# Kernel optimization log

Measured on AMD Instinct MI355X. Metric: run time of the kernel, lower is better.

## Reference

```python
import jax, jax.numpy as jnp
import numpy as np

INPUT_SCALE = 1.0
TABLE_SIZE = 32
D_EMBED = 64
N = 1_000_000


def setup_inputs() -> dict:
    key = jax.random.key(0)
    k1, k2 = jax.random.split(key)
    x = jax.random.normal(k1, (N, 3), dtype=jnp.float32)
    # learned table parameter: [E, D, H, W] (batch dim of 1 dropped)
    table = jax.random.normal(k2, (D_EMBED, TABLE_SIZE, TABLE_SIZE, TABLE_SIZE), dtype=jnp.float32) * 0.1
    return {"x": x, "table": table}


def _grid_sample_3d(table, grid):
    """F.grid_sample(table[None], grid[None,None,None]) with mode='bilinear',
    padding_mode='zeros', align_corners=False.
    table: [E, D, H, W]; grid: [n, 3] with (x->W, y->H, z->D) order.
    Returns [n, E]."""
    E, Dz, Hy, Wx = table.shape
    sizes_f = jnp.array([Wx, Hy, Dz], dtype=table.dtype)
    dims_i = jnp.array([Wx, Hy, Dz], dtype=jnp.int32)
    # align_corners=False: pix = ((coord + 1) * size - 1) / 2
    pix = ((grid + 1.0) * sizes_f - 1.0) * 0.5   # [n, 3]
    p0f = jnp.floor(pix)
    frac = pix - p0f                              # [n, 3]
    p0 = p0f.astype(jnp.int32)
    tab_flat = table.reshape(E, -1).T             # [D*H*W, E]
    out = jnp.zeros((grid.shape[0], E), dtype=table.dtype)
    for dz in (0, 1):
        for dy in (0, 1):
            for dx in (0, 1):
                off = jnp.array([dx, dy, dz], dtype=jnp.int32)
                idx = p0 + off                                        # [n, 3]
                inb = jnp.all((idx >= 0) & (idx < dims_i), axis=-1)   # zeros padding
                idxc = jnp.clip(idx, 0, dims_i - 1)
                lin = (idxc[:, 2] * Hy + idxc[:, 1]) * Wx + idxc[:, 0]
                vals = tab_flat[lin]                                  # [n, E]
                w = jnp.prod(jnp.where(off == 1, frac, 1.0 - frac), axis=-1)
                out = out + vals * (w * inb.astype(table.dtype))[:, None]
    return out


def reference(x, table):
    xc = jnp.clip(x * INPUT_SCALE, -1.0, 1.0)
    return _grid_sample_3d(table, xc)
```

## Files before the change

### kernel.cpp

```cpp
#include <hip/hip_runtime.h>


constexpr int TSZ = 32;
constexpr int S   = TSZ * TSZ * TSZ;
constexpr int EMB = 64;

typedef float        floatx4 __attribute__((ext_vector_type(4)));
typedef float        f32x2   __attribute__((ext_vector_type(2)));

__device__ __forceinline__ unsigned short f32_to_bf16_rne(float f) {
  unsigned int u = __float_as_uint(f);
  unsigned int lsb = (u >> 16) & 1u;
  u += 0x7FFFu + lsb;
  return (unsigned short)(u >> 16);
}

__global__ __launch_bounds__(256) void transpose_table_k(
    const float* __restrict__ tab, unsigned short* __restrict__ tabT) {
  __shared__ float tile[EMB][EMB + 1];
  const int s_base = blockIdx.x * 64;
  const int t  = threadIdx.x;
  const int c0 = t & 63;
  const int r0 = t >> 6;
#pragma unroll
  for (int i = 0; i < 16; ++i) {
    const int e = r0 + 4 * i;
    tile[e][c0] = tab[(size_t)e * S + (s_base + c0)];
  }
  __syncthreads();
#pragma unroll
  for (int i = 0; i < 16; ++i) {
    const int s = r0 + 4 * i;
    tabT[(size_t)(s_base + s) * EMB + c0] = f32_to_bf16_rne(tile[c0][s]);
  }
}

__global__ __launch_bounds__(256) void embed_k(
    const float* __restrict__ x, const uint4* __restrict__ tabT,
    float* __restrict__ out, int n) {
  const int gid = blockIdx.x * 256 + threadIdx.x;
  const int pt  = gid >> 3;
  if (pt >= n) return;
  const int c8 = gid & 7;

  const float gx = fminf(fmaxf(__builtin_nontemporal_load(&x[3 * pt + 0]), -1.f), 1.f);
  const float gy = fminf(fmaxf(__builtin_nontemporal_load(&x[3 * pt + 1]), -1.f), 1.f);
  const float gz = fminf(fmaxf(__builtin_nontemporal_load(&x[3 * pt + 2]), -1.f), 1.f);
  const float px = ((gx + 1.f) * 32.f - 1.f) * 0.5f;
  const float py = ((gy + 1.f) * 32.f - 1.f) * 0.5f;
  const float pz = ((gz + 1.f) * 32.f - 1.f) * 0.5f;

  const float fxf = floorf(px), fyf = floorf(py), fzf = floorf(pz);
  const int ix0 = (int)fxf, iy0 = (int)fyf, iz0 = (int)fzf;
  const float fx = px - fxf, fy = py - fyf, fz = pz - fzf;

  float wxe[2], wye[2], wze[2];
  int   ixc[2], iyc[2], izc[2];
  wxe[0] = (ix0 >= 0)      ? (1.f - fx) : 0.f;
  wxe[1] = (ix0 + 1 < TSZ) ? fx         : 0.f;
  ixc[0] = max(ix0, 0);
  ixc[1] = min(ix0 + 1, TSZ - 1);
  wye[0] = (iy0 >= 0)      ? (1.f - fy) : 0.f;
  wye[1] = (iy0 + 1 < TSZ) ? fy         : 0.f;
  iyc[0] = max(iy0, 0);
  iyc[1] = min(iy0 + 1, TSZ - 1);
  wze[0] = (iz0 >= 0)      ? (1.f - fz) : 0.f;
  wze[1] = (iz0 + 1 < TSZ) ? fz         : 0.f;
  izc[0] = max(iz0, 0);
  izc[1] = min(iz0 + 1, TSZ - 1);

  f32x2 a01 = {0.f, 0.f}, a23 = {0.f, 0.f}, a45 = {0.f, 0.f}, a67 = {0.f, 0.f};

#pragma unroll
  for (int dz = 0; dz < 2; ++dz) {
    const int zb = izc[dz] * (TSZ * TSZ);
#pragma unroll
    for (int dy = 0; dy < 2; ++dy) {
      const int   zyb = zb + iyc[dy] * TSZ;
      const float wzy = wze[dz] * wye[dy];
#pragma unroll
      for (int dx = 0; dx < 2; ++dx) {
        const float w   = wzy * wxe[dx];
        const int   lin = zyb + ixc[dx];
        const uint4 q   = tabT[lin * 8 + c8];
        const f32x2 w2  = {w, w};
        const f32x2 v01 = {__uint_as_float(q.x << 16),
                           __uint_as_float(q.x & 0xFFFF0000u)};
        const f32x2 v23 = {__uint_as_float(q.y << 16),
                           __uint_as_float(q.y & 0xFFFF0000u)};
        const f32x2 v45 = {__uint_as_float(q.z << 16),
                           __uint_as_float(q.z & 0xFFFF0000u)};
        const f32x2 v67 = {__uint_as_float(q.w << 16),
                           __uint_as_float(q.w & 0xFFFF0000u)};
        a01 = __builtin_elementwise_fma(v01, w2, a01);
        a23 = __builtin_elementwise_fma(v23, w2, a23);
        a45 = __builtin_elementwise_fma(v45, w2, a45);
        a67 = __builtin_elementwise_fma(v67, w2, a67);
      }
    }
  }

  const float accv[8] = {a01.x, a01.y, a23.x, a23.y, a45.x, a45.y, a67.x, a67.y};
  const int lane = threadIdx.x & 63;
  const int grp  = lane & ~7;
  const int src1 = grp + (c8 >> 1);
  const int src2 = grp + 4 + (c8 >> 1);
  const bool hi  = (c8 & 1) != 0;
  float o0[4], o1[4];
#pragma unroll
  for (int j = 0; j < 4; ++j) {
    const float aj = __shfl(accv[j],     src1, 64);
    const float bj = __shfl(accv[4 + j], src1, 64);
    o0[j] = hi ? bj : aj;
    const float cj = __shfl(accv[j],     src2, 64);
    const float dj = __shfl(accv[4 + j], src2, 64);
    o1[j] = hi ? dj : cj;
  }
  const floatx4 s0 = {o0[0], o0[1], o0[2], o0[3]};
  const floatx4 s1 = {o1[0], o1[1], o1[2], o1[3]};
  float* rowp = out + (size_t)pt * EMB;
  *(floatx4*)(rowp + c8 * 4)      = s0;
  *(floatx4*)(rowp + 32 + c8 * 4) = s1;
}

__global__ __launch_bounds__(256) void embed_fallback_k(
    const float* __restrict__ x, const float* __restrict__ tab,
    float* __restrict__ out, int n) {
  const int gid = blockIdx.x * 256 + threadIdx.x;
  const int pt  = gid >> 6;
  if (pt >= n) return;
  const int e = gid & 63;

  const float gx = fminf(fmaxf(x[3 * pt + 0], -1.f), 1.f);
  const float gy = fminf(fmaxf(x[3 * pt + 1], -1.f), 1.f);
  const float gz = fminf(fmaxf(x[3 * pt + 2], -1.f), 1.f);
  const float px = ((gx + 1.f) * 32.f - 1.f) * 0.5f;
  const float py = ((gy + 1.f) * 32.f - 1.f) * 0.5f;
  const float pz = ((gz + 1.f) * 32.f - 1.f) * 0.5f;

  const float fxf = floorf(px), fyf = floorf(py), fzf = floorf(pz);
  const int ix0 = (int)fxf, iy0 = (int)fyf, iz0 = (int)fzf;
  const float fx = px - fxf, fy = py - fyf, fz = pz - fzf;
  const float wx[2] = {1.f - fx, fx};
  const float wy[2] = {1.f - fy, fy};
  const float wz[2] = {1.f - fz, fz};

  float acc = 0.f;
#pragma unroll
  for (int dz = 0; dz < 2; ++dz) {
    const int  iz  = iz0 + dz;
    const bool bz  = (unsigned)iz < (unsigned)TSZ;
    const int  izc = min(max(iz, 0), TSZ - 1);
#pragma unroll
    for (int dy = 0; dy < 2; ++dy) {
      const int  iy  = iy0 + dy;
      const bool by  = (unsigned)iy < (unsigned)TSZ;
      const int  iyc = min(max(iy, 0), TSZ - 1);
#pragma unroll
      for (int dx = 0; dx < 2; ++dx) {
        const int  ix  = ix0 + dx;
        const bool bx  = (unsigned)ix < (unsigned)TSZ;
        const int  ixc = min(max(ix, 0), TSZ - 1);
        float w = wz[dz] * wy[dy] * wx[dx];
        w = (bx && by && bz) ? w : 0.f;
        const int lin = (izc * TSZ + iyc) * TSZ + ixc;
        acc = fmaf(w, tab[(size_t)e * S + lin], acc);
      }
    }
  }
  out[(size_t)pt * EMB + e] = acc;
}

extern "C" void kernel_launch(void* const* d_in, const int* in_sizes, int n_in,
                              void* d_out, int out_size, void* d_ws,
                              size_t ws_size, hipStream_t stream) {
  const float* x   = (const float*)d_in[0];
  const float* tab = (const float*)d_in[1];
  float*       out = (float*)d_out;
  const int n = in_sizes[0] / 3;

  const size_t need = (size_t)S * EMB * sizeof(unsigned short);
  if (ws_size >= need) {
    unsigned short* tabT = (unsigned short*)d_ws;
    transpose_table_k<<<S / 64, 256, 0, stream>>>(tab, tabT);
    const int total  = n * 8;
    const int blocks = (total + 255) / 256;
    embed_k<<<blocks, 256, 0, stream>>>(x, (const uint4*)tabT, out, n);
  } else {
    const int total  = n * EMB;
    const int blocks = (total + 255) / 256;
    embed_fallback_k<<<blocks, 256, 0, stream>>>(x, tab, out, n);
  }
}
```

Before: 313.9 us.

## Quantize transposed table to int8 with per-channel scales for gathers

Adds a per-channel absmax pass and stores the transposed table as offset int8 (128-biased) instead of bf16. The embed kernel gathers 8 bytes per lane per corner, accumulates the weighted unsigned values, and then subtracts the bias and applies the scale, which halves table gather bytes. Output stores are switched to nontemporal. This adds an extra small kernel launch and lowers table precision to 8 bits, which may exceed the accuracy tolerance.

```diff
diff --git a/kernel.cpp b/kernel.cpp
--- a/kernel.cpp
+++ b/kernel.cpp
@@ -5,18 +5,28 @@
 constexpr int S   = TSZ * TSZ * TSZ;
 constexpr int EMB = 64;
 
-typedef float        floatx4 __attribute__((ext_vector_type(4)));
-typedef float        f32x2   __attribute__((ext_vector_type(2)));
-
-__device__ __forceinline__ unsigned short f32_to_bf16_rne(float f) {
-  unsigned int u = __float_as_uint(f);
-  unsigned int lsb = (u >> 16) & 1u;
-  u += 0x7FFFu + lsb;
-  return (unsigned short)(u >> 16);
-}
-
-__global__ __launch_bounds__(256) void transpose_table_k(
-    const float* __restrict__ tab, unsigned short* __restrict__ tabT) {
+typedef float floatx4 __attribute__((ext_vector_type(4)));
+
+__global__ __launch_bounds__(256) void amax_k(
+    const float* __restrict__ tab, float* __restrict__ scale) {
+  __shared__ float red[256];
+  const int ch = blockIdx.x;
+  const int t  = threadIdx.x;
+  float m = 0.f;
+  for (int i = 0; i < S / 256; ++i)
+    m = fmaxf(m, fabsf(tab[(size_t)ch * S + t + 256 * i]));
+  red[t] = m;
+  __syncthreads();
+  for (int off = 128; off > 0; off >>= 1) {
+    if (t < off) red[t] = fmaxf(red[t], red[t + off]);
+    __syncthreads();
+  }
+  if (t == 0) scale[ch] = fmaxf(red[0], 1e-30f) * (1.0f / 127.0f);
+}
+
+__global__ __launch_bounds__(256) void transpose_quant_k(
+    const float* __restrict__ tab, const float* __restrict__ scale,
+    unsigned char* __restrict__ tabQ) {
   __shared__ float tile[EMB][EMB + 1];
   const int s_base = blockIdx.x * 64;
   const int t  = threadIdx.x;
@@ -28,16 +38,18 @@
     tile[e][c0] = tab[(size_t)e * S + (s_base + c0)];
   }
   __syncthreads();
+  const float rs = 1.0f / scale[c0];
 #pragma unroll
   for (int i = 0; i < 16; ++i) {
     const int s = r0 + 4 * i;
-    tabT[(size_t)(s_base + s) * EMB + c0] = f32_to_bf16_rne(tile[c0][s]);
-  }
-}
-
-__global__ __launch_bounds__(256) void embed_k(
-    const float* __restrict__ x, const uint4* __restrict__ tabT,
-    float* __restrict__ out, int n) {
+    const int q = __float2int_rn(tile[c0][s] * rs) + 128;
+    tabQ[(size_t)(s_base + s) * EMB + c0] = (unsigned char)q;
+  }
+}
+
+__global__ __launch_bounds__(256) void embed_q_k(
+    const float* __restrict__ x, const unsigned char* __restrict__ tabQ,
+    const float* __restrict__ scale, float* __restrict__ out, int n) {
   const int gid = blockIdx.x * 256 + threadIdx.x;
   const int pt  = gid >> 3;
   if (pt >= n) return;
@@ -69,7 +81,9 @@
   izc[0] = max(iz0, 0);
   izc[1] = min(iz0 + 1, TSZ - 1);
 
-  f32x2 a01 = {0.f, 0.f}, a23 = {0.f, 0.f}, a45 = {0.f, 0.f}, a67 = {0.f, 0.f};
+  float a0 = 0.f, a1 = 0.f, a2 = 0.f, a3 = 0.f;
+  float a4 = 0.f, a5 = 0.f, a6 = 0.f, a7 = 0.f;
+  float sumw = 0.f;
 
 #pragma unroll
   for (int dz = 0; dz < 2; ++dz) {
@@ -82,25 +96,28 @@
       for (int dx = 0; dx < 2; ++dx) {
         const float w   = wzy * wxe[dx];
         const int   lin = zyb + ixc[dx];
-        const uint4 q   = tabT[lin * 8 + c8];
-        const f32x2 w2  = {w, w};
-        const f32x2 v01 = {__uint_as_float(q.x << 16),
-                           __uint_as_float(q.x & 0xFFFF0000u)};
-        const f32x2 v23 = {__uint_as_float(q.y << 16),
-                           __uint_as_float(q.y & 0xFFFF0000u)};
-        const f32x2 v45 = {__uint_as_float(q.z << 16),
-                           __uint_as_float(q.z & 0xFFFF0000u)};
-        const f32x2 v67 = {__uint_as_float(q.w << 16),
-                           __uint_as_float(q.w & 0xFFFF0000u)};
-        a01 = __builtin_elementwise_fma(v01, w2, a01);
-        a23 = __builtin_elementwise_fma(v23, w2, a23);
-        a45 = __builtin_elementwise_fma(v45, w2, a45);
-        a67 = __builtin_elementwise_fma(v67, w2, a67);
+        const uint2 q   = *(const uint2*)(tabQ + (size_t)lin * EMB + c8 * 8);
+        sumw += w;
+        a0 = fmaf(w, (float)(q.x & 0xFFu),         a0);
+        a1 = fmaf(w, (float)((q.x >> 8)  & 0xFFu), a1);
+        a2 = fmaf(w, (float)((q.x >> 16) & 0xFFu), a2);
+        a3 = fmaf(w, (float)((q.x >> 24) & 0xFFu), a3);
+        a4 = fmaf(w, (float)(q.y & 0xFFu),         a4);
+        a5 = fmaf(w, (float)((q.y >> 8)  & 0xFFu), a5);
+        a6 = fmaf(w, (float)((q.y >> 16) & 0xFFu), a6);
+        a7 = fmaf(w, (float)((q.y >> 24) & 0xFFu), a7);
       }
     }
   }
 
-  const float accv[8] = {a01.x, a01.y, a23.x, a23.y, a45.x, a45.y, a67.x, a67.y};
+  const float m128 = 128.0f * sumw;
+  const floatx4 sA = *(const floatx4*)(scale + c8 * 8);
+  const floatx4 sB = *(const floatx4*)(scale + c8 * 8 + 4);
+  const float accv[8] = {sA.x * (a0 - m128), sA.y * (a1 - m128),
+                         sA.z * (a2 - m128), sA.w * (a3 - m128),
+                         sB.x * (a4 - m128), sB.y * (a5 - m128),
+                         sB.z * (a6 - m128), sB.w * (a7 - m128)};
+
   const int lane = threadIdx.x & 63;
   const int grp  = lane & ~7;
   const int src1 = grp + (c8 >> 1);
@@ -119,8 +136,8 @@
   const floatx4 s0 = {o0[0], o0[1], o0[2], o0[3]};
   const floatx4 s1 = {o1[0], o1[1], o1[2], o1[3]};
   float* rowp = out + (size_t)pt * EMB;
-  *(floatx4*)(rowp + c8 * 4)      = s0;
-  *(floatx4*)(rowp + 32 + c8 * 4) = s1;
+  __builtin_nontemporal_store(s0, (floatx4*)(rowp + c8 * 4));
+  __builtin_nontemporal_store(s1, (floatx4*)(rowp + 32 + c8 * 4));
 }
 
 __global__ __launch_bounds__(256) void embed_fallback_k(
@@ -179,13 +196,16 @@
   float*       out = (float*)d_out;
   const int n = in_sizes[0] / 3;
 
-  const size_t need = (size_t)S * EMB * sizeof(unsigned short);
+  const size_t off_tabq = 256;
+  const size_t need = off_tabq + (size_t)S * EMB;
   if (ws_size >= need) {
-    unsigned short* tabT = (unsigned short*)d_ws;
-    transpose_table_k<<<S / 64, 256, 0, stream>>>(tab, tabT);
+    float*         scale = (float*)d_ws;
+    unsigned char* tabQ  = (unsigned char*)d_ws + off_tabq;
+    amax_k<<<EMB, 256, 0, stream>>>(tab, scale);
+    transpose_quant_k<<<S / 64, 256, 0, stream>>>(tab, scale, tabQ);
     const int total  = n * 8;
     const int blocks = (total + 255) / 256;
-    embed_k<<<blocks, 256, 0, stream>>>(x, (const uint4*)tabT, out, n);
+    embed_q_k<<<blocks, 256, 0, stream>>>(x, tabQ, scale, out, n);
   } else {
     const int total  = n * EMB;
     const int blocks = (total + 255) / 256;
```

After: 336.8 us. 7.3% more time.

## Use four threads per point with 16 contiguous channels each, drop shuffles

Applied to the files above, without the earlier changes.

Each point is now handled by four threads instead of eight. Each thread loads two consecutive 16-byte bf16 chunks per corner, so it owns 16 contiguous output channels and writes them with four float4 stores. This removes the cross-lane shuffle transpose and halves the per-point coordinate and weight computation. In exchange each thread holds more registers, and the stores are less coalesced because each thread writes a 64-byte span.

```diff
diff --git a/kernel.cpp b/kernel.cpp
--- a/kernel.cpp
+++ b/kernel.cpp
@@ -5,8 +5,8 @@
 constexpr int S   = TSZ * TSZ * TSZ;
 constexpr int EMB = 64;
 
-typedef float        floatx4 __attribute__((ext_vector_type(4)));
-typedef float        f32x2   __attribute__((ext_vector_type(2)));
+typedef float floatx4 __attribute__((ext_vector_type(4)));
+typedef float f32x2   __attribute__((ext_vector_type(2)));
 
 __device__ __forceinline__ unsigned short f32_to_bf16_rne(float f) {
   unsigned int u = __float_as_uint(f);
@@ -39,9 +39,9 @@
     const float* __restrict__ x, const uint4* __restrict__ tabT,
     float* __restrict__ out, int n) {
   const int gid = blockIdx.x * 256 + threadIdx.x;
-  const int pt  = gid >> 3;
+  const int pt  = gid >> 2;
   if (pt >= n) return;
-  const int c8 = gid & 7;
+  const int o = gid & 3;
 
   const float gx = fminf(fmaxf(__builtin_nontemporal_load(&x[3 * pt + 0]), -1.f), 1.f);
   const float gy = fminf(fmaxf(__builtin_nontemporal_load(&x[3 * pt + 1]), -1.f), 1.f);
@@ -69,7 +69,8 @@
   izc[0] = max(iz0, 0);
   izc[1] = min(iz0 + 1, TSZ - 1);
 
-  f32x2 a01 = {0.f, 0.f}, a23 = {0.f, 0.f}, a45 = {0.f, 0.f}, a67 = {0.f, 0.f};
+  f32x2 a0 = {0.f, 0.f}, a1 = {0.f, 0.f}, a2 = {0.f, 0.f}, a3 = {0.f, 0.f};
+  f32x2 a4 = {0.f, 0.f}, a5 = {0.f, 0.f}, a6 = {0.f, 0.f}, a7 = {0.f, 0.f};
 
 #pragma unroll
   for (int dz = 0; dz < 2; ++dz) {
@@ -82,45 +83,47 @@
       for (int dx = 0; dx < 2; ++dx) {
         const float w   = wzy * wxe[dx];
         const int   lin = zyb + ixc[dx];
-        const uint4 q   = tabT[lin * 8 + c8];
+        const uint4* rp = &tabT[lin * 8 + o * 2];
+        const uint4 qa  = rp[0];
+        const uint4 qb  = rp[1];
         const f32x2 w2  = {w, w};
-        const f32x2 v01 = {__uint_as_float(q.x << 16),
-                           __uint_as_float(q.x & 0xFFFF0000u)};
-        const f32x2 v23 = {__uint_as_float(q.y << 16),
-                           __uint_as_float(q.y & 0xFFFF0000u)};
-        const f32x2 v45 = {__uint_as_float(q.z << 16),
-                           __uint_as_float(q.z & 0xFFFF0000u)};
-        const f32x2 v67 = {__uint_as_float(q.w << 16),
-                           __uint_as_float(q.w & 0xFFFF0000u)};
-        a01 = __builtin_elementwise_fma(v01, w2, a01);
-        a23 = __builtin_elementwise_fma(v23, w2, a23);
-        a45 = __builtin_elementwise_fma(v45, w2, a45);
-        a67 = __builtin_elementwise_fma(v67, w2, a67);
+        const f32x2 vA0 = {__uint_as_float(qa.x << 16),
+                           __uint_as_float(qa.x & 0xFFFF0000u)};
+        const f32x2 vA1 = {__uint_as_float(qa.y << 16),
+                           __uint_as_float(qa.y & 0xFFFF0000u)};
+        const f32x2 vA2 = {__uint_as_float(qa.z << 16),
+                           __uint_as_float(qa.z & 0xFFFF0000u)};
+        const f32x2 vA3 = {__uint_as_float(qa.w << 16),
+                           __uint_as_float(qa.w & 0xFFFF0000u)};
+        const f32x2 vB0 = {__uint_as_float(qb.x << 16),
+                           __uint_as_float(qb.x & 0xFFFF0000u)};
+        const f32x2 vB1 = {__uint_as_float(qb.y << 16),
+                           __uint_as_float(qb.y & 0xFFFF0000u)};
+        const f32x2 vB2 = {__uint_as_float(qb.z << 16),
+                           __uint_as_float(qb.z & 0xFFFF0000u)};
+        const f32x2 vB3 = {__uint_as_float(qb.w << 16),
+                           __uint_as_float(qb.w & 0xFFFF0000u)};
+        a0 = __builtin_elementwise_fma(vA0, w2, a0);
+        a1 = __builtin_elementwise_fma(vA1, w2, a1);
+        a2 = __builtin_elementwise_fma(vA2, w2, a2);
+        a3 = __builtin_elementwise_fma(vA3, w2, a3);
+        a4 = __builtin_elementwise_fma(vB0, w2, a4);
+        a5 = __builtin_elementwise_fma(vB1, w2, a5);
+        a6 = __builtin_elementwise_fma(vB2, w2, a6);
+        a7 = __builtin_elementwise_fma(vB3, w2, a7);
       }
     }
   }
 
-  const float accv[8] = {a01.x, a01.y, a23.x, a23.y, a45.x, a45.y, a67.x, a67.y};
-  const int lane = threadIdx.x & 63;
-  const int grp  = lane & ~7;
-  const int src1 = grp + (c8 >> 1);
-  const int src2 = grp + 4 + (c8 >> 1);
-  const bool hi  = (c8 & 1) != 0;
-  float o0[4], o1[4];
-#pragma unroll
-  for (int j = 0; j < 4; ++j) {
-    const float aj = __shfl(accv[j],     src1, 64);
-    const float bj = __shfl(accv[4 + j], src1, 64);
-    o0[j] = hi ? bj : aj;
-    const float cj = __shfl(accv[j],     src2, 64);
-    const float dj = __shfl(accv[4 + j], src2, 64);
-    o1[j] = hi ? dj : cj;
-  }
-  const floatx4 s0 = {o0[0], o0[1], o0[2], o0[3]};
-  const floatx4 s1 = {o1[0], o1[1], o1[2], o1[3]};
-  float* rowp = out + (size_t)pt * EMB;
-  *(floatx4*)(rowp + c8 * 4)      = s0;
-  *(floatx4*)(rowp + 32 + c8 * 4) = s1;
+  float* rowp = out + (size_t)pt * EMB + o * 16;
+  const floatx4 s0 = {a0.x, a0.y, a1.x, a1.y};
+  const floatx4 s1 = {a2.x, a2.y, a3.x, a3.y};
+  const floatx4 s2 = {a4.x, a4.y, a5.x, a5.y};
+  const floatx4 s3 = {a6.x, a6.y, a7.x, a7.y};
+  *(floatx4*)(rowp + 0)  = s0;
+  *(floatx4*)(rowp + 4)  = s1;
+  *(floatx4*)(rowp + 8)  = s2;
+  *(floatx4*)(rowp + 12) = s3;
 }
 
 __global__ __launch_bounds__(256) void embed_fallback_k(
@@ -183,7 +186,7 @@
   if (ws_size >= need) {
     unsigned short* tabT = (unsigned short*)d_ws;
     transpose_table_k<<<S / 64, 256, 0, stream>>>(tab, tabT);
-    const int total  = n * 8;
+    const int total  = n * 4;
     const int blocks = (total + 255) / 256;
     embed_k<<<blocks, 256, 0, stream>>>(x, (const uint4*)tabT, out, n);
   } else {
```

New measurement: 333.8 us. 6.3% more time.
